# Kernel tuning notes

Measured on AMD Instinct MI355X. Metric: run time of the kernel, lower is better.

The kernel has to match this reference:

```python
import jax, jax.numpy as jnp
import numpy as np

B, T, IN, H, OUT = 64, 2048, 64, 512, 32


def setup_inputs() -> dict:
    key = jax.random.key(0)
    ks = jax.random.split(key, 8)
    # xavier_normal with gain=0.5: std = gain * sqrt(2/(fan_in+fan_out))
    std_fz = 0.5 * np.sqrt(2.0 / ((IN + H) + 2 * H))
    std_r = 0.5 * np.sqrt(2.0 / ((IN + H) + H))
    # nn.Linear default init: uniform(-1/sqrt(fan_in), 1/sqrt(fan_in))
    lim = 1.0 / np.sqrt(H)
    return {
        "u": jax.random.normal(ks[0], (B, T, IN), dtype=jnp.float32),
        "x0": jax.random.uniform(ks[1], (B, 1, H), dtype=jnp.float32),
        "kernel_fz": std_fz * jax.random.normal(ks[2], (IN + H, 2 * H), dtype=jnp.float32),
        "bias_fz": jnp.zeros((2 * H,), dtype=jnp.float32),
        "kernel_r": std_r * jax.random.normal(ks[3], (IN + H, H), dtype=jnp.float32),
        "bias_r": jnp.zeros((H,), dtype=jnp.float32),
        "W_out": jax.random.uniform(ks[4], (OUT, H), dtype=jnp.float32, minval=-lim, maxval=lim),
        "b_out": jax.random.uniform(ks[5], (OUT,), dtype=jnp.float32, minval=-lim, maxval=lim),
    }


def reference(u, x0, kernel_fz, bias_fz, kernel_r, bias_r, W_out, b_out):
    Hd = kernel_r.shape[1]
    x_init = x0[:, 0, :]  # [B, H]

    def step(x, u_t):
        # u_t: [B, IN], x: [B, H]
        fz = jax.nn.sigmoid(jnp.concatenate([u_t, x], axis=-1) @ kernel_fz + bias_fz)
        f, z = fz[:, :Hd], fz[:, Hd:]
        r = jnp.tanh(jnp.concatenate([u_t, f * x], axis=-1) @ kernel_r + bias_r)
        xk = (1.0 - z) * x + z * r
        y = x @ W_out.T + b_out  # output computed from PREVIOUS state, as in torch step()
        return xk, y

    u_tb = jnp.swapaxes(u, 0, 1)  # [T, B, IN]
    _, ys = jax.lax.scan(step, x_init, u_tb)  # ys: [T, B, OUT]
    return jnp.swapaxes(ys, 0, 1)  # [B, T, OUT]
```

## Files before the change

kernel.cpp:

```cpp
#include <hip/hip_runtime.h>
#include <stdint.h>

#define B_    64
#define T_    2048
#define IN_   64
#define H_    512
#define H2_   1024
#define OUT_  32
#define KTOT  576

#define NBG   8
#define NCG   32
#define NTHR  256
#define BPG   8
#define KSL   18
#define RS    12

#define ABORT_IDX 0
#define BUF_BASE  16
#define PAIRS_BG  (H_ * BPG)
#define PSLAB     (NBG * PAIRS_BG * 2)

__device__ __forceinline__ void gpub2(float* p, float v, unsigned e) {
  unsigned long long q =
      ((unsigned long long)e << 32) | (unsigned long long)__float_as_uint(v);
  asm volatile("global_atomic_swap_x2 %0, %1, off sc1"
               :: "v"(p), "v"(q) : "memory");
}

__device__ __forceinline__ bool poll_slab(
    const float* b0, const float* b1, unsigned target, unsigned* abort_w,
    float4& r0, float4& r1, float4& r2, float4& r3,
    float4& r4, float4& r5, float4& r6, float4& r7) {
  int polls = 0;
  for (;;) {
    asm volatile(
        "global_load_dwordx4 %0, %8, off sc0 sc1\n\t"
        "global_load_dwordx4 %1, %8, off offset:16 sc0 sc1\n\t"
        "global_load_dwordx4 %2, %8, off offset:32 sc0 sc1\n\t"
        "global_load_dwordx4 %3, %8, off offset:48 sc0 sc1\n\t"
        "global_load_dwordx4 %4, %9, off sc0 sc1\n\t"
        "global_load_dwordx4 %5, %9, off offset:16 sc0 sc1\n\t"
        "global_load_dwordx4 %6, %9, off offset:32 sc0 sc1\n\t"
        "global_load_dwordx4 %7, %9, off offset:48 sc0 sc1\n\t"
        "s_waitcnt vmcnt(0)"
        : "=&v"(r0), "=&v"(r1), "=&v"(r2), "=&v"(r3),
          "=&v"(r4), "=&v"(r5), "=&v"(r6), "=&v"(r7)
        : "v"(b0), "v"(b1)
        : "memory");
    unsigned m =
        (__float_as_uint(r0.y) ^ target) | (__float_as_uint(r0.w) ^ target) |
        (__float_as_uint(r1.y) ^ target) | (__float_as_uint(r1.w) ^ target) |
        (__float_as_uint(r2.y) ^ target) | (__float_as_uint(r2.w) ^ target) |
        (__float_as_uint(r3.y) ^ target) | (__float_as_uint(r3.w) ^ target) |
        (__float_as_uint(r4.y) ^ target) | (__float_as_uint(r4.w) ^ target) |
        (__float_as_uint(r5.y) ^ target) | (__float_as_uint(r5.w) ^ target) |
        (__float_as_uint(r6.y) ^ target) | (__float_as_uint(r6.w) ^ target) |
        (__float_as_uint(r7.y) ^ target) | (__float_as_uint(r7.w) ^ target);
    if (m == 0u) return true;
    __builtin_amdgcn_s_sleep(1);
    if ((++polls & 63) == 0) {
      if (__hip_atomic_load(abort_w, __ATOMIC_RELAXED, __HIP_MEMORY_SCOPE_AGENT) != 0u ||
          polls > 300000) {
        __hip_atomic_store(abort_w, 1u, __ATOMIC_RELAXED, __HIP_MEMORY_SCOPE_AGENT);
        return false;
      }
    }
  }
}

__global__ __launch_bounds__(256) void gru_init(float* ws, const float* __restrict__ x0) {
  int i = blockIdx.x * blockDim.x + threadIdx.x;
  int stride = gridDim.x * blockDim.x;
  unsigned* w = (unsigned*)ws;
  for (int k = i; k < BUF_BASE; k += stride) w[k] = 0u;
  unsigned* rest = w + BUF_BASE + PSLAB;
  for (int k = i; k < 2 * PSLAB; k += stride) rest[k] = 0u;
  for (int p = i; p < NBG * PAIRS_BG; p += stride) {
    int bg = p >> 12, col = (p >> 3) & (H_ - 1), b = p & 7;
    ws[BUF_BASE + 2 * p] = x0[(bg * 8 + b) * H_ + col];
    w[BUF_BASE + 2 * p + 1] = 0u;
  }
}

__global__ __launch_bounds__(NTHR, 1) void gru_main(
    const float* __restrict__ u, const float* __restrict__ kfz,
    const float* __restrict__ bfz, const float* __restrict__ kr,
    const float* __restrict__ br, const float* __restrict__ wout,
    const float* __restrict__ bout, float* __restrict__ out, float* ws) {
  unsigned* abort_w = (unsigned*)ws + ABORT_IDX;
  float* xg0p = ws + BUF_BASE;
  float* xg1p = xg0p + PSLAB;
  float* xfgp = xg1p + PSLAB;

  const int bg  = blockIdx.x & 7;
  const int cg  = blockIdx.x >> 3;
  const int tid = threadIdx.x;
  const int w   = tid >> 6;
  const int l   = tid & 63;
  const int cq  = l & 7;
  const int g   = l >> 3;
  const int kb  = (w * 8 + g) * KSL;
  const int fc  = tid >> 3;
  const int fb  = tid & 7;
  const int yb  = tid >> 5;
  const int yq  = tid & 31;

  __shared__ float bufA[KTOT * RS];
  __shared__ float pA[4 * 32 * RS];
  __shared__ float pB[4 * 16 * RS];
  __shared__ float rbuf[16 * 8];
  __shared__ int s_bad;

  float wA[KSL][4];
#pragma unroll
  for (int i = 0; i < KSL; ++i)
#pragma unroll
    for (int m = 0; m < 4; ++m) {
      int c = 4 * cq + m;
      int gcol = (c < 16) ? (16 * cg + c) : (512 + 16 * cg + (c - 16));
      wA[i][m] = kfz[(size_t)(kb + i) * H2_ + gcol];
    }
  float wB[KSL][2];
#pragma unroll
  for (int i = 0; i < KSL; ++i)
#pragma unroll
    for (int m = 0; m < 2; ++m)
      wB[i][m] = kr[(size_t)(kb + i) * H_ + (16 * cg + 2 * cq + m)];
  float wy[16];
#pragma unroll
  for (int i = 0; i < 16; ++i) wy[i] = wout[cg * H_ + (yq + 32 * i)];
  const float by = bout[cg];
  const int fzc = (fc < 16) ? (16 * cg + fc) : (512 + 16 * cg + (fc - 16));
  const float biasA = bfz[fzc];
  const float biasB = (tid < 128) ? br[16 * cg + fc] : 0.0f;

  float zreg = 0.0f, xoldz = 0.0f;

  if (tid == 0) s_bad = 0;
  {
    int k2 = tid & 31, b = tid >> 5;
    float2 uv = *(const float2*)&u[((size_t)(bg * 8 + b) * T_) * IN_ + 2 * k2];
    bufA[(2 * k2) * RS + b] = uv.x;
    bufA[(2 * k2 + 1) * RS + b] = uv.y;
  }
  __syncthreads();

  for (int t = 0; t < T_; ++t) {
    const float* xcp = (t & 1) ? xg1p : xg0p;
    float*       xnp = (t & 1) ? xg0p : xg1p;

    {
      const float* b0 = xcp + 2 * ((size_t)bg * PAIRS_BG + (size_t)tid * 8);
      const float* b1 = b0 + 4096;
      float4 r0, r1, r2, r3, r4, r5, r6, r7;
      bool ok = poll_slab(b0, b1, (unsigned)t, abort_w,
                          r0, r1, r2, r3, r4, r5, r6, r7);
      if (!ok) s_bad = 1;
      __syncthreads();
      if (s_bad) return;
      *(float4*)&bufA[(64 + tid) * RS]       = make_float4(r0.x, r0.z, r1.x, r1.z);
      *(float4*)&bufA[(64 + tid) * RS + 4]   = make_float4(r2.x, r2.z, r3.x, r3.z);
      *(float4*)&bufA[(64 + tid + 256) * RS]     = make_float4(r4.x, r4.z, r5.x, r5.z);
      *(float4*)&bufA[(64 + tid + 256) * RS + 4] = make_float4(r6.x, r6.z, r7.x, r7.z);
    }
    __syncthreads();

    float acc[4][8] = {};
#pragma unroll
    for (int i = 0; i < KSL; ++i) {
      const float* xr = &bufA[(kb + i) * RS];
      float4 x0 = *(const float4*)xr;
      float4 x1 = *(const float4*)(xr + 4);
#pragma unroll
      for (int m = 0; m < 4; ++m) {
        float wv = wA[i][m];
        acc[m][0] += wv * x0.x; acc[m][1] += wv * x0.y;
        acc[m][2] += wv * x0.z; acc[m][3] += wv * x0.w;
        acc[m][4] += wv * x1.x; acc[m][5] += wv * x1.y;
        acc[m][6] += wv * x1.z; acc[m][7] += wv * x1.w;
      }
    }

#pragma unroll
    for (int m = 0; m < 4; ++m)
#pragma unroll
      for (int b = 0; b < 8; ++b) {
        acc[m][b] += __shfl_xor(acc[m][b], 8);
        acc[m][b] += __shfl_xor(acc[m][b], 16);
        acc[m][b] += __shfl_xor(acc[m][b], 32);
      }
    if (g == 0) {
#pragma unroll
      for (int m = 0; m < 4; ++m) {
        float* p = &pA[(w * 32 + 4 * cq + m) * RS];
        *(float4*)p = make_float4(acc[m][0], acc[m][1], acc[m][2], acc[m][3]);
        *(float4*)(p + 4) = make_float4(acc[m][4], acc[m][5], acc[m][6], acc[m][7]);
      }
    }
    __syncthreads();

    {
      float s = pA[(0 * 32 + fc) * RS + fb] + pA[(1 * 32 + fc) * RS + fb] +
                pA[(2 * 32 + fc) * RS + fb] + pA[(3 * 32 + fc) * RS + fb] + biasA;
      float sig = 1.0f / (1.0f + __expf(-s));
      if (fc < 16) {
        float xo = bufA[(64 + 16 * cg + fc) * RS + fb];
        float* p = &xfgp[2 * ((size_t)bg * PAIRS_BG + (size_t)(16 * cg + fc) * 8 + fb)];
        gpub2(p, sig * xo, (unsigned)(t + 1));
      } else {
        zreg = sig;
        xoldz = bufA[(64 + 16 * cg + (fc - 16)) * RS + fb];
      }
    }

    {
      float yp = 0.0f;
#pragma unroll
      for (int i = 0; i < 16; ++i)
        yp += wy[i] * bufA[(64 + yq + 32 * i) * RS + yb];
      yp += __shfl_xor(yp, 1);  yp += __shfl_xor(yp, 2);
      yp += __shfl_xor(yp, 4);  yp += __shfl_xor(yp, 8);
      yp += __shfl_xor(yp, 16);
      if (yq == 0)
        out[((size_t)(bg * 8 + yb) * T_ + t) * OUT_ + cg] = yp + by;
    }

    {
      const float* b0 = xfgp + 2 * ((size_t)bg * PAIRS_BG + (size_t)tid * 8);
      const float* b1 = b0 + 4096;
      float4 r0, r1, r2, r3, r4, r5, r6, r7;
      bool ok = poll_slab(b0, b1, (unsigned)(t + 1), abort_w,
                          r0, r1, r2, r3, r4, r5, r6, r7);
      if (!ok) s_bad = 1;
      __syncthreads();
      if (s_bad) return;
      *(float4*)&bufA[(64 + tid) * RS]       = make_float4(r0.x, r0.z, r1.x, r1.z);
      *(float4*)&bufA[(64 + tid) * RS + 4]   = make_float4(r2.x, r2.z, r3.x, r3.z);
      *(float4*)&bufA[(64 + tid + 256) * RS]     = make_float4(r4.x, r4.z, r5.x, r5.z);
      *(float4*)&bufA[(64 + tid + 256) * RS + 4] = make_float4(r6.x, r6.z, r7.x, r7.z);
    }
    __syncthreads();

    float acc2[2][8] = {};
#pragma unroll
    for (int i = 0; i < KSL; ++i) {
      const float* xr = &bufA[(kb + i) * RS];
      float4 x0 = *(const float4*)xr;
      float4 x1 = *(const float4*)(xr + 4);
#pragma unroll
      for (int m = 0; m < 2; ++m) {
        float wv = wB[i][m];
        acc2[m][0] += wv * x0.x; acc2[m][1] += wv * x0.y;
        acc2[m][2] += wv * x0.z; acc2[m][3] += wv * x0.w;
        acc2[m][4] += wv * x1.x; acc2[m][5] += wv * x1.y;
        acc2[m][6] += wv * x1.z; acc2[m][7] += wv * x1.w;
      }
    }
#pragma unroll
    for (int m = 0; m < 2; ++m)
#pragma unroll
      for (int b = 0; b < 8; ++b) {
        acc2[m][b] += __shfl_xor(acc2[m][b], 8);
        acc2[m][b] += __shfl_xor(acc2[m][b], 16);
        acc2[m][b] += __shfl_xor(acc2[m][b], 32);
      }
    if (g == 0) {
#pragma unroll
      for (int m = 0; m < 2; ++m) {
        float* p = &pB[(w * 16 + 2 * cq + m) * RS];
        *(float4*)p = make_float4(acc2[m][0], acc2[m][1], acc2[m][2], acc2[m][3]);
        *(float4*)(p + 4) = make_float4(acc2[m][4], acc2[m][5], acc2[m][6], acc2[m][7]);
      }
    }
    __syncthreads();

    if (tid < 128) {
      float s = pB[(0 * 16 + fc) * RS + fb] + pB[(1 * 16 + fc) * RS + fb] +
                pB[(2 * 16 + fc) * RS + fb] + pB[(3 * 16 + fc) * RS + fb] + biasB;
      float e = __expf(2.0f * s);
      rbuf[fc * 8 + fb] = 1.0f - 2.0f / (1.0f + e);
    }
    __syncthreads();

    if (tid >= 128) {
      float r = rbuf[(fc - 16) * 8 + fb];
      float xn = xoldz + zreg * (r - xoldz);
      float* p = &xnp[2 * ((size_t)bg * PAIRS_BG + (size_t)(16 * cg + (fc - 16)) * 8 + fb)];
      gpub2(p, xn, (unsigned)(t + 1));
    }
    if (t + 1 < T_) {
      int k2 = tid & 31, b = tid >> 5;
      float2 uv = *(const float2*)&u[((size_t)(bg * 8 + b) * T_ + (t + 1)) * IN_ + 2 * k2];
      bufA[(2 * k2) * RS + b] = uv.x;
      bufA[(2 * k2 + 1) * RS + b] = uv.y;
    }
  }
}

extern "C" void kernel_launch(void* const* d_in, const int* in_sizes, int n_in,
                              void* d_out, int out_size, void* d_ws, size_t ws_size,
                              hipStream_t stream) {
  const float* u    = (const float*)d_in[0];
  const float* x0   = (const float*)d_in[1];
  const float* kfz  = (const float*)d_in[2];
  const float* bfz  = (const float*)d_in[3];
  const float* kr   = (const float*)d_in[4];
  const float* br   = (const float*)d_in[5];
  const float* wout = (const float*)d_in[6];
  const float* bout = (const float*)d_in[7];
  float* out = (float*)d_out;
  float* ws  = (float*)d_ws;

  hipLaunchKernelGGL(gru_init, dim3(64), dim3(256), 0, stream, ws, x0);
  hipLaunchKernelGGL(gru_main, dim3(NBG * NCG), dim3(NTHR), 0, stream,
                     u, kfz, bfz, kr, br, wout, bout, out, ws);
}
```

Before: 15.85 ms.

## Gate slab polling behind per-block step flags

Adds a small array of padded per-block progress flags. Each column-group block publishes a step counter after writing its gate or state slice. Before each phase, 32 threads poll those flags as a barrier, and only then is the tagged 64-bit slab read. The aim is to cut the heavy polling of large slabs by every thread while data is not yet ready. The cost is an extra flag round trip and a __syncthreads per phase on the critical path of a latency-bound recurrence.

```diff
diff --git a/kernel.cpp b/kernel.cpp
--- a/kernel.cpp
+++ b/kernel.cpp
@@ -16,16 +16,29 @@
 #define KSL   18
 #define RS    12
 
-#define ABORT_IDX 0
-#define BUF_BASE  16
-#define PAIRS_BG  (H_ * BPG)
-#define PSLAB     (NBG * PAIRS_BG * 2)
+#define FLAG_STRIDE 16
+#define ABORT_IDX   0
+#define FLAGS_OFF   16
+#define FLAG_WORDS  (NBG * 2 * NCG * FLAG_STRIDE)
+#define BUF_BASE    (FLAGS_OFF + FLAG_WORDS)
+#define PAIRS_BG    (H_ * BPG)
+#define PSLAB       (NBG * PAIRS_BG * 2)
 
 __device__ __forceinline__ void gpub2(float* p, float v, unsigned e) {
   unsigned long long q =
       ((unsigned long long)e << 32) | (unsigned long long)__float_as_uint(v);
   asm volatile("global_atomic_swap_x2 %0, %1, off sc1"
                :: "v"(p), "v"(q) : "memory");
+}
+__device__ __forceinline__ void gpubu(unsigned* p, unsigned v) {
+  asm volatile("global_atomic_swap %0, %1, off sc1"
+               :: "v"(p), "v"(v) : "memory");
+}
+__device__ __forceinline__ unsigned gpollu(const unsigned* p) {
+  unsigned v;
+  asm volatile("global_load_dword %0, %1, off sc0 sc1\n\ts_waitcnt vmcnt(0)"
+               : "=v"(v) : "v"(p) : "memory");
+  return v;
 }
 
 __device__ __forceinline__ bool poll_slab(
@@ -61,12 +74,41 @@
     __builtin_amdgcn_s_sleep(1);
     if ((++polls & 63) == 0) {
       if (__hip_atomic_load(abort_w, __ATOMIC_RELAXED, __HIP_MEMORY_SCOPE_AGENT) != 0u ||
-          polls > 300000) {
+          polls > 500000) {
         __hip_atomic_store(abort_w, 1u, __ATOMIC_RELAXED, __HIP_MEMORY_SCOPE_AGENT);
         return false;
       }
     }
   }
+}
+
+__device__ __forceinline__ bool gbar_wait(unsigned* base, unsigned target,
+                                          unsigned* abort_w) {
+  __shared__ int s_ok;
+  const int tid = threadIdx.x;
+  int ok = 1;
+  if (tid < NCG) {
+    const unsigned* f = base + tid * FLAG_STRIDE;
+    int polls = 0;
+    while (gpollu(f) < target) {
+      __builtin_amdgcn_s_sleep(1);
+      if ((++polls & 255) == 0) {
+        if (__hip_atomic_load(abort_w, __ATOMIC_RELAXED, __HIP_MEMORY_SCOPE_AGENT) != 0u ||
+            polls > 2000000) {
+          __hip_atomic_store(abort_w, 1u, __ATOMIC_RELAXED, __HIP_MEMORY_SCOPE_AGENT);
+          ok = 0;
+          break;
+        }
+      }
+    }
+  }
+  if (tid < 64) {
+    unsigned long long bad = __ballot(ok == 0);
+    if (tid == 0) s_ok = (bad == 0ull) ? 1 : 0;
+  }
+  __syncthreads();
+  __atomic_signal_fence(__ATOMIC_ACQUIRE);
+  return s_ok != 0;
 }
 
 __global__ __launch_bounds__(256) void gru_init(float* ws, const float* __restrict__ x0) {
@@ -88,7 +130,9 @@
     const float* __restrict__ bfz, const float* __restrict__ kr,
     const float* __restrict__ br, const float* __restrict__ wout,
     const float* __restrict__ bout, float* __restrict__ out, float* ws) {
-  unsigned* abort_w = (unsigned*)ws + ABORT_IDX;
+  unsigned* wsu = (unsigned*)ws;
+  unsigned* flags = wsu + FLAGS_OFF;
+  unsigned* abort_w = wsu + ABORT_IDX;
   float* xg0p = ws + BUF_BASE;
   float* xg1p = xg0p + PSLAB;
   float* xfgp = xg1p + PSLAB;
@@ -106,6 +150,11 @@
   const int yb  = tid >> 5;
   const int yq  = tid & 31;
 
+  unsigned* slotA = flags + ((bg * 2 + 0) * NCG + cg) * FLAG_STRIDE;
+  unsigned* slotB = flags + ((bg * 2 + 1) * NCG + cg) * FLAG_STRIDE;
+  unsigned* baseA = flags + (bg * 2 + 0) * NCG * FLAG_STRIDE;
+  unsigned* baseB = flags + (bg * 2 + 1) * NCG * FLAG_STRIDE;
+
   __shared__ float bufA[KTOT * RS];
   __shared__ float pA[4 * 32 * RS];
   __shared__ float pB[4 * 16 * RS];
@@ -150,6 +199,7 @@
     const float* xcp = (t & 1) ? xg1p : xg0p;
     float*       xnp = (t & 1) ? xg0p : xg1p;
 
+    if (!gbar_wait(baseB, (unsigned)t, abort_w)) return;
     {
       const float* b0 = xcp + 2 * ((size_t)bg * PAIRS_BG + (size_t)tid * 8);
       const float* b1 = b0 + 4096;
@@ -208,6 +258,7 @@
         float xo = bufA[(64 + 16 * cg + fc) * RS + fb];
         float* p = &xfgp[2 * ((size_t)bg * PAIRS_BG + (size_t)(16 * cg + fc) * 8 + fb)];
         gpub2(p, sig * xo, (unsigned)(t + 1));
+        if (tid == 0) gpubu(slotA, (unsigned)(t + 1));
       } else {
         zreg = sig;
         xoldz = bufA[(64 + 16 * cg + (fc - 16)) * RS + fb];
@@ -226,6 +277,7 @@
         out[((size_t)(bg * 8 + yb) * T_ + t) * OUT_ + cg] = yp + by;
     }
 
+    if (!gbar_wait(baseA, (unsigned)(t + 1), abort_w)) return;
     {
       const float* b0 = xfgp + 2 * ((size_t)bg * PAIRS_BG + (size_t)tid * 8);
       const float* b1 = b0 + 4096;
@@ -288,7 +340,9 @@
       float xn = xoldz + zreg * (r - xoldz);
       float* p = &xnp[2 * ((size_t)bg * PAIRS_BG + (size_t)(16 * cg + (fc - 16)) * 8 + fb)];
       gpub2(p, xn, (unsigned)(t + 1));
-    }
+      if (tid == 128) gpubu(slotB, (unsigned)(t + 1));
+    }
+
     if (t + 1 < T_) {
       int k2 = tid & 31, b = tid >> 5;
       float2 uv = *(const float2*)&u[((size_t)(bg * 8 + b) * T_ + (t + 1)) * IN_ + 2 * k2];
```

Result: slower. 17.74 ms (+11.9%).
